# Kernel optimization log

Hardware: AMD Instinct MI355X
Metric: run time of the kernel (lower is better)

## Reference

```python
import jax, jax.numpy as jnp
import numpy as np

TAU = 2.0
EPS_COH = 1e-8
EPS_NLL = 1e-7
ALPHA = 0.0
# component-vs-modality mask: rows = (common, synergy, g_spec, p_spec), cols = (gene, path)
MASK = np.array([[1.0, 1.0], [0.0, 0.0], [1.0, 0.0], [0.0, 1.0]], dtype=np.float32)


def l2norm(x, axis=-1):
    n = jnp.sqrt(jnp.sum(x * x, axis=axis, keepdims=True))
    return x / jnp.maximum(n, 1e-12)


def setup_inputs() -> dict:
    key = jax.random.key(0)
    ks = jax.random.split(key, 8)
    B, K, C, N = 64, 4, 256, 8192
    hazards = jax.random.uniform(ks[0], (B, K), dtype=jnp.float32)
    S = jnp.cumprod(1.0 - hazards, axis=1)  # survival curve, matches torch semantics
    indiv = jax.random.normal(ks[1], (B, 4, C), dtype=jnp.float32)
    gene = jax.random.normal(ks[2], (B, 1, C), dtype=jnp.float32)
    path = jax.random.normal(ks[3], (B, 1, C), dtype=jnp.float32)
    cohort_bank = jax.random.normal(ks[4], (K, N, 4, C), dtype=jnp.float32)
    label = jax.random.randint(ks[5], (B,), 0, K).astype(jnp.int32)
    c = jax.random.randint(ks[6], (B,), 0, 2).astype(jnp.int32)
    return {"hazards": hazards, "S": S, "indiv": indiv, "gene": gene,
            "path": path, "cohort_bank": cohort_bank, "label": label, "c": c}


def reference(hazards, S, indiv, gene, path, cohort_bank, label, c):
    B, K = hazards.shape
    dt = hazards.dtype
    # ---- NLLSurvLoss ----
    cf = c.astype(dt)[:, None]                       # [B,1] censoring flag
    Y = label.astype(jnp.int32)[:, None]             # [B,1]
    S_padded = jnp.concatenate([jnp.ones((B, 1), dt), S], axis=1)  # [B,K+1]
    s_y = jnp.take_along_axis(S_padded, Y, axis=1)
    h_y = jnp.take_along_axis(hazards, Y, axis=1)
    s_y1 = jnp.take_along_axis(S_padded, Y + 1, axis=1)
    clamp = lambda x: jnp.maximum(x, EPS_NLL)
    uncensored = -(1.0 - cf) * (jnp.log(clamp(s_y)) + jnp.log(clamp(h_y)))
    censored = -cf * jnp.log(clamp(s_y1))
    neg_l = censored + uncensored
    nll = ((1.0 - ALPHA) * neg_l + ALPHA * uncensored).mean()
    # ---- CohortLoss: intra ----
    indiv_n = l2norm(indiv)                          # [B,4,C]
    gp_n = l2norm(jnp.concatenate([gene, path], axis=1))  # [B,2,C]
    sim = jnp.einsum('bpc,btc->bpt', indiv_n, gp_n)  # [B,4,2]
    mask = jnp.asarray(MASK, dtype=dt)               # [4,2]
    intra = (jnp.abs(sim) * (1.0 - mask) - mask * sim).mean(axis=(1, 2)) + 1.0
    intra_loss = intra.mean()
    # ---- CohortLoss: inter (vectorized cohort-bank retrieval) ----
    n_cls, N = cohort_bank.shape[0], cohort_bank.shape[1]
    anchors = l2norm(indiv.mean(axis=1))             # [B,C]
    bank_means = cohort_bank.mean(axis=2)            # [n_cls,N,C]
    bank_n = l2norm(bank_means)                      # [n_cls,N,C]
    sims = jnp.einsum('knc,bc->bkn', bank_n, anchors)  # [B,n_cls,N]
    e = jnp.exp(sims / TAU)
    pos_mask = (label[:, None] == jnp.arange(n_cls, dtype=label.dtype)[None, :]).astype(dt)[:, :, None]  # [B,n_cls,1]
    ep = jnp.sum(e * pos_mask) / (B * N)                       # mean over B*N positive sims
    en = jnp.sum(e * (1.0 - pos_mask)) / (B * (n_cls - 1) * N)  # mean over B*(n_cls-1)*N negative sims
    inter_loss = -jnp.log((ep + EPS_COH) / (ep + en + EPS_COH))
    cohort_loss = intra_loss + inter_loss
    # Loss_factory: total = 1.0*nllsurv + 1.0*cohort
    return nll + cohort_loss
```

## Files before the change

### kernel.cpp

```cpp
#include <hip/hip_runtime.h>
#include <math.h>

#define BB 64
#define KK 4
#define CC 256
#define NN 8192
#define NROWS (KK*NN)
#define GRID_NORM 2048
#define GRID_INTER 512
#define WPG 4

#define WS_BN_OFF    0
#define WS_B_OFF     16777216
#define WS_SLOT_OFF  16809984
#define WS_NLL_OFF   16818176
#define WS_INTRA_OFF 16818432
#define WS_TKT_OFF   16818688

#define EPS_NLL 1e-7f

typedef __attribute__((ext_vector_type(8))) short bf16x8;
typedef __attribute__((ext_vector_type(4))) float f32x4;

__device__ __forceinline__ float4 f4add(float4 a, float4 b){ return make_float4(a.x+b.x, a.y+b.y, a.z+b.z, a.w+b.w); }
__device__ __forceinline__ float4 f4scale(float4 a, float s){ return make_float4(a.x*s, a.y*s, a.z*s, a.w*s); }
__device__ __forceinline__ float dot4(float4 a, float4 b){ return a.x*b.x + a.y*b.y + a.z*b.z + a.w*b.w; }

__device__ __forceinline__ float wred(float v){
#pragma unroll
  for (int m = 32; m >= 1; m >>= 1) v += __shfl_xor(v, m, 64);
  return v;
}

__device__ __forceinline__ unsigned short f2bf(float x){
  union { float f; unsigned u; } v; v.f = x;
  unsigned r = v.u + 0x7fffu + ((v.u >> 16) & 1u);
  return (unsigned short)(r >> 16);
}

__global__ __launch_bounds__(64) void prep_kernel(
    const float* __restrict__ hazards, const float* __restrict__ S,
    const float* __restrict__ indiv,   const float* __restrict__ gene,
    const float* __restrict__ path,    const int* __restrict__ label,
    const int* __restrict__ cvec,      char* __restrict__ ws)
{
  const int b = blockIdx.x;
  const int lane = threadIdx.x;

  const float4* ind4 = (const float4*)indiv + (size_t)b * 256;
  float4 i0 = ind4[  0 + lane];
  float4 i1 = ind4[ 64 + lane];
  float4 i2 = ind4[128 + lane];
  float4 i3 = ind4[192 + lane];
  float4 g  = ((const float4*)gene)[b*64 + lane];
  float4 p  = ((const float4*)path)[b*64 + lane];

  float4 am = f4scale(f4add(f4add(i0, i1), f4add(i2, i3)), 0.25f);
  float na = sqrtf(wred(dot4(am, am)));
  float4 an = f4scale(am, 1.0f / fmaxf(na, 1e-12f));

  {
    const int cq = lane;
    const unsigned addr = (unsigned)((cq >> 3) * 4096
                        + (b >> 4) * 1024
                        + ((((cq >> 1) & 3) * 16) + (b & 15)) * 16
                        + (cq & 1) * 8);
    ushort4 h4;
    h4.x = f2bf(an.x); h4.y = f2bf(an.y); h4.z = f2bf(an.z); h4.w = f2bf(an.w);
    *(ushort4*)(ws + WS_B_OFF + addr) = h4;
  }

  float4 v[6] = {i0, i1, i2, i3, g, p};
#pragma unroll
  for (int j = 0; j < 6; ++j) {
    float n = sqrtf(wred(dot4(v[j], v[j])));
    v[j] = f4scale(v[j], 1.0f / fmaxf(n, 1e-12f));
  }

  float s[4][2];
#pragma unroll
  for (int pp = 0; pp < 4; ++pp)
#pragma unroll
    for (int t = 0; t < 2; ++t)
      s[pp][t] = wred(dot4(v[pp], v[4+t]));

  if (lane == 0) {
    float intra = (-s[0][0]) + (-s[0][1])
                + fabsf(s[1][0]) + fabsf(s[1][1])
                + (-s[2][0]) + fabsf(s[2][1])
                + fabsf(s[3][0]) + (-s[3][1]);
    intra = intra * 0.125f + 1.0f;
    ((float*)(ws + WS_INTRA_OFF))[b] = intra;

    int   Y  = label[b];
    float cf = (float)cvec[b];
    float s_y  = (Y == 0) ? 1.0f : S[b*KK + Y - 1];
    float s_y1 = S[b*KK + Y];
    float h_y  = hazards[b*KK + Y];
    float neg_l = -cf * logf(fmaxf(s_y1, EPS_NLL))
                  - (1.0f - cf) * (logf(fmaxf(s_y, EPS_NLL)) + logf(fmaxf(h_y, EPS_NLL)));
    ((float*)(ws + WS_NLL_OFF))[b] = neg_l;
  }
}

__global__ __launch_bounds__(256, 4) void bank_norm_kernel(
    const float* __restrict__ bank, char* __restrict__ ws)
{
  const int tid  = threadIdx.x;
  const int wave = tid >> 6;
  const int lane = tid & 63;
  const int gw   = blockIdx.x * WPG + wave;
  const int row0 = gw * 4;

  const float4* b4 = (const float4*)bank;
  ushort4* bn = (ushort4*)(ws + WS_BN_OFF);

  float4 r[4][4];
#pragma unroll
  for (int rr = 0; rr < 4; ++rr)
#pragma unroll
    for (int c = 0; c < 4; ++c)
      r[rr][c] = b4[(size_t)(row0 + rr) * 256 + c * 64 + lane];

#pragma unroll
  for (int rr = 0; rr < 4; ++rr) {
    float4 m = f4add(f4add(r[rr][0], r[rr][1]), f4add(r[rr][2], r[rr][3]));
    float ss = wred(dot4(m, m));
    float rs = rsqrtf(fmaxf(ss, 1e-24f));
    ushort4 h4;
    h4.x = f2bf(m.x * rs); h4.y = f2bf(m.y * rs);
    h4.z = f2bf(m.z * rs); h4.w = f2bf(m.w * rs);
    bn[(size_t)(row0 + rr) * 64 + lane] = h4;
  }
}

__global__ __launch_bounds__(256) void inter_kernel(
    const int* __restrict__ label, char* __restrict__ ws, float* __restrict__ out)
{
  __shared__ uint4 Bl[2048];
  __shared__ double redw[WPG][2];
  __shared__ unsigned tkt_s;

  const int tid  = threadIdx.x;
  const int wave = tid >> 6;
  const int lane = tid & 63;
  const int lm   = lane & 15;
  const int lg   = lane >> 4;

  const uint4* Bg = (const uint4*)(ws + WS_B_OFF);
#pragma unroll
  for (int i = 0; i < 8; ++i) Bl[tid + i*256] = Bg[tid + i*256];
  __syncthreads();

  const int gw   = blockIdx.x * WPG + wave;
  const int row0 = gw * 16;
  const int kk   = row0 >> 13;

  int lab[4];
#pragma unroll
  for (int nt = 0; nt < 4; ++nt) lab[nt] = label[nt*16 + lm];

  const short* bnp = (const short*)(ws + WS_BN_OFF) + (size_t)(row0 + lm) * 256 + lg * 8;
  bf16x8 af[8];
#pragma unroll
  for (int kc = 0; kc < 8; ++kc)
    af[kc] = *(const bf16x8*)(bnp + kc * 32);

  f32x4 acc0 = {0,0,0,0}, acc1 = {0,0,0,0}, acc2 = {0,0,0,0}, acc3 = {0,0,0,0};
#pragma unroll
  for (int kc = 0; kc < 8; ++kc) {
    acc0 = __builtin_amdgcn_mfma_f32_16x16x32_bf16(af[kc], *(const bf16x8*)&Bl[(kc*4+0)*64 + lane], acc0, 0, 0, 0);
    acc1 = __builtin_amdgcn_mfma_f32_16x16x32_bf16(af[kc], *(const bf16x8*)&Bl[(kc*4+1)*64 + lane], acc1, 0, 0, 0);
    acc2 = __builtin_amdgcn_mfma_f32_16x16x32_bf16(af[kc], *(const bf16x8*)&Bl[(kc*4+2)*64 + lane], acc2, 0, 0, 0);
    acc3 = __builtin_amdgcn_mfma_f32_16x16x32_bf16(af[kc], *(const bf16x8*)&Bl[(kc*4+3)*64 + lane], acc3, 0, 0, 0);
  }

  float epf = 0.0f, enf = 0.0f;
#define DO_NT(ACC, NT)                                                        \
  {                                                                           \
    float es = expf(ACC.x * 0.5f) + expf(ACC.y * 0.5f)                        \
             + expf(ACC.z * 0.5f) + expf(ACC.w * 0.5f);                       \
    if (lab[NT] == kk) epf += es; else enf += es;                             \
  }
  DO_NT(acc0, 0) DO_NT(acc1, 1) DO_NT(acc2, 2) DO_NT(acc3, 3)
#undef DO_NT

  epf = wred(epf);
  enf = wred(enf);
  if (lane == 0) {
    redw[wave][0] = (double)epf;
    redw[wave][1] = (double)enf;
  }
  __syncthreads();

  double*   slots  = (double*)(ws + WS_SLOT_OFF);
  unsigned* ticket = (unsigned*)(ws + WS_TKT_OFF);

  if (tid == 0) {
    double bep = 0.0, ben = 0.0;
#pragma unroll
    for (int w = 0; w < WPG; ++w) { bep += redw[w][0]; ben += redw[w][1]; }
    slots[blockIdx.x*2 + 0] = bep;
    slots[blockIdx.x*2 + 1] = ben;
    __threadfence();
    tkt_s = atomicAdd(ticket, 1u);
  }
  __syncthreads();

  if (tkt_s == GRID_INTER - 1 && wave == 0) {
    __threadfence();
    double pep = 0.0, pen = 0.0;
    for (int i = lane; i < GRID_INTER; i += 64) {
      pep += slots[2*i + 0];
      pen += slots[2*i + 1];
    }
#pragma unroll
    for (int m = 32; m >= 1; m >>= 1) {
      pep += __shfl_xor(pep, m, 64);
      pen += __shfl_xor(pen, m, 64);
    }
    float scal = ((const float*)(ws + WS_NLL_OFF))[lane]
               + ((const float*)(ws + WS_INTRA_OFF))[lane];
    scal = wred(scal);
    if (lane == 0) {
      double ep = pep / (double)(BB * NN);
      double en = pen / (double)(BB * (KK-1) * NN);
      double inter = -log((ep + 1e-8) / (ep + en + 1e-8));
      out[0] = (float)((double)scal / 64.0 + inter);
    }
  }
}

extern "C" void kernel_launch(void* const* d_in, const int* in_sizes, int n_in,
                              void* d_out, int out_size, void* d_ws, size_t ws_size,
                              hipStream_t stream)
{
  const float* hazards = (const float*)d_in[0];
  const float* S       = (const float*)d_in[1];
  const float* indiv   = (const float*)d_in[2];
  const float* gene    = (const float*)d_in[3];
  const float* path    = (const float*)d_in[4];
  const float* bank    = (const float*)d_in[5];
  const int*   label   = (const int*)d_in[6];
  const int*   cvec    = (const int*)d_in[7];
  char*  ws  = (char*)d_ws;
  float* out = (float*)d_out;

  hipMemsetAsync(ws + WS_TKT_OFF, 0, 4, stream);
  prep_kernel<<<dim3(BB), dim3(64), 0, stream>>>(hazards, S, indiv, gene, path, label, cvec, ws);
  bank_norm_kernel<<<dim3(GRID_NORM), dim3(256), 0, stream>>>(bank, ws);
  inter_kernel<<<dim3(GRID_INTER), dim3(256), 0, stream>>>(label, ws, out);
}
```

Measured before the change: 229.7 us.

## Fuse bank normalization into inter kernel via per-wave LDS staging

Merges the cohort-bank mean/normalize pass into the MFMA similarity kernel. Each wave loads 16 bank rows in four passes, normalizes them and writes bf16 into a swizzled per-wave LDS tile, which then feeds the MFMA A operand directly. This drops the 16 MB bf16 intermediate write and re-read plus one kernel launch. In exchange, only 512 blocks must stream the 128 MB bank, with more LDS per block and an occupancy hint of 2, which may reduce memory-level parallelism.

```diff
diff --git a/kernel.cpp b/kernel.cpp
--- a/kernel.cpp
+++ b/kernel.cpp
@@ -6,16 +6,14 @@
 #define CC 256
 #define NN 8192
 #define NROWS (KK*NN)
-#define GRID_NORM 2048
-#define GRID_INTER 512
+#define GRID_F 512
 #define WPG 4
 
-#define WS_BN_OFF    0
-#define WS_B_OFF     16777216
-#define WS_SLOT_OFF  16809984
-#define WS_NLL_OFF   16818176
-#define WS_INTRA_OFF 16818432
-#define WS_TKT_OFF   16818688
+#define WS_B_OFF     0
+#define WS_SLOT_OFF  32768
+#define WS_NLL_OFF   40960
+#define WS_INTRA_OFF 41216
+#define WS_TKT_OFF   41472
 
 #define EPS_NLL 1e-7f
 
@@ -103,41 +101,12 @@
   }
 }
 
-__global__ __launch_bounds__(256, 4) void bank_norm_kernel(
-    const float* __restrict__ bank, char* __restrict__ ws)
-{
-  const int tid  = threadIdx.x;
-  const int wave = tid >> 6;
-  const int lane = tid & 63;
-  const int gw   = blockIdx.x * WPG + wave;
-  const int row0 = gw * 4;
-
-  const float4* b4 = (const float4*)bank;
-  ushort4* bn = (ushort4*)(ws + WS_BN_OFF);
-
-  float4 r[4][4];
-#pragma unroll
-  for (int rr = 0; rr < 4; ++rr)
-#pragma unroll
-    for (int c = 0; c < 4; ++c)
-      r[rr][c] = b4[(size_t)(row0 + rr) * 256 + c * 64 + lane];
-
-#pragma unroll
-  for (int rr = 0; rr < 4; ++rr) {
-    float4 m = f4add(f4add(r[rr][0], r[rr][1]), f4add(r[rr][2], r[rr][3]));
-    float ss = wred(dot4(m, m));
-    float rs = rsqrtf(fmaxf(ss, 1e-24f));
-    ushort4 h4;
-    h4.x = f2bf(m.x * rs); h4.y = f2bf(m.y * rs);
-    h4.z = f2bf(m.z * rs); h4.w = f2bf(m.w * rs);
-    bn[(size_t)(row0 + rr) * 64 + lane] = h4;
-  }
-}
-
-__global__ __launch_bounds__(256) void inter_kernel(
-    const int* __restrict__ label, char* __restrict__ ws, float* __restrict__ out)
+__global__ __launch_bounds__(256, 2) void fused_kernel(
+    const float* __restrict__ bank, const int* __restrict__ label,
+    char* __restrict__ ws, float* __restrict__ out)
 {
   __shared__ uint4 Bl[2048];
+  __shared__ uint4 At4[WPG][512];
   __shared__ double redw[WPG][2];
   __shared__ unsigned tkt_s;
 
@@ -155,16 +124,42 @@
   const int gw   = blockIdx.x * WPG + wave;
   const int row0 = gw * 16;
   const int kk   = row0 >> 13;
+  char* At = (char*)&At4[wave][0];
 
   int lab[4];
 #pragma unroll
   for (int nt = 0; nt < 4; ++nt) lab[nt] = label[nt*16 + lm];
 
-  const short* bnp = (const short*)(ws + WS_BN_OFF) + (size_t)(row0 + lm) * 256 + lg * 8;
+  const float4* b4 = (const float4*)bank;
+
+#pragma unroll 1
+  for (int pass = 0; pass < 4; ++pass) {
+    const int rp0 = row0 + pass * 4;
+
+    float4 r[4][4];
+#pragma unroll
+    for (int rr = 0; rr < 4; ++rr)
+#pragma unroll
+      for (int c = 0; c < 4; ++c)
+        r[rr][c] = b4[(size_t)(rp0 + rr) * 256 + c * 64 + lane];
+
+#pragma unroll
+    for (int rr = 0; rr < 4; ++rr) {
+      float4 m = f4add(f4add(r[rr][0], r[rr][1]), f4add(r[rr][2], r[rr][3]));
+      float ss = wred(dot4(m, m));
+      float rs = rsqrtf(fmaxf(ss, 1e-24f));
+      const int lr = pass * 4 + rr;
+      ushort4 h4;
+      h4.x = f2bf(m.x * rs); h4.y = f2bf(m.y * rs);
+      h4.z = f2bf(m.z * rs); h4.w = f2bf(m.w * rs);
+      *(ushort4*)(At + lr*512 + ((lane*8) ^ ((lr & 7) << 4))) = h4;
+    }
+  }
+
   bf16x8 af[8];
 #pragma unroll
   for (int kc = 0; kc < 8; ++kc)
-    af[kc] = *(const bf16x8*)(bnp + kc * 32);
+    af[kc] = *(const bf16x8*)(At + lm*512 + ((kc*64 + lg*16) ^ ((lm & 7) << 4)));
 
   f32x4 acc0 = {0,0,0,0}, acc1 = {0,0,0,0}, acc2 = {0,0,0,0}, acc3 = {0,0,0,0};
 #pragma unroll
@@ -207,10 +202,10 @@
   }
   __syncthreads();
 
-  if (tkt_s == GRID_INTER - 1 && wave == 0) {
+  if (tkt_s == GRID_F - 1 && wave == 0) {
     __threadfence();
     double pep = 0.0, pen = 0.0;
-    for (int i = lane; i < GRID_INTER; i += 64) {
+    for (int i = lane; i < GRID_F; i += 64) {
       pep += slots[2*i + 0];
       pen += slots[2*i + 1];
     }
@@ -248,6 +243,5 @@
 
   hipMemsetAsync(ws + WS_TKT_OFF, 0, 4, stream);
   prep_kernel<<<dim3(BB), dim3(64), 0, stream>>>(hazards, S, indiv, gene, path, label, cvec, ws);
-  bank_norm_kernel<<<dim3(GRID_NORM), dim3(256), 0, stream>>>(bank, ws);
-  inter_kernel<<<dim3(GRID_INTER), dim3(256), 0, stream>>>(label, ws, out);
-}
+  fused_kernel<<<dim3(GRID_F), dim3(256), 0, stream>>>(bank, label, ws, out);
+}
```

New measurement: 234.5 us. 2.1% more time.

## Write normalized bank in MFMA-fragment layout and halve rows per wave

Applied to the files above, without the earlier changes.

The bank normalization kernel now handles two rows per wave instead of four, doubles its grid and raises the occupancy hint. It stores the bf16 normalized rows in a tiled layout that matches the MFMA A-fragment order. The inter kernel can then read each fragment as a contiguous 16-byte-per-lane load instead of strided row reads. The intent is more memory parallelism in the bandwidth-bound 128MB bank read and coalesced fragment loads in the GEMM stage.

```diff
diff --git a/kernel.cpp b/kernel.cpp
--- a/kernel.cpp
+++ b/kernel.cpp
@@ -6,7 +6,7 @@
 #define CC 256
 #define NN 8192
 #define NROWS (KK*NN)
-#define GRID_NORM 2048
+#define GRID_NORM 4096
 #define GRID_INTER 512
 #define WPG 4
 
@@ -103,35 +103,48 @@
   }
 }
 
-__global__ __launch_bounds__(256, 4) void bank_norm_kernel(
+__global__ __launch_bounds__(256, 8) void norm_stream_kernel(
     const float* __restrict__ bank, char* __restrict__ ws)
 {
   const int tid  = threadIdx.x;
   const int wave = tid >> 6;
   const int lane = tid & 63;
   const int gw   = blockIdx.x * WPG + wave;
-  const int row0 = gw * 4;
+  const int row0 = gw * 2;
 
   const float4* b4 = (const float4*)bank;
-  ushort4* bn = (ushort4*)(ws + WS_BN_OFF);
-
-  float4 r[4][4];
-#pragma unroll
-  for (int rr = 0; rr < 4; ++rr)
-#pragma unroll
-    for (int c = 0; c < 4; ++c)
-      r[rr][c] = b4[(size_t)(row0 + rr) * 256 + c * 64 + lane];
-
-#pragma unroll
-  for (int rr = 0; rr < 4; ++rr) {
-    float4 m = f4add(f4add(r[rr][0], r[rr][1]), f4add(r[rr][2], r[rr][3]));
-    float ss = wred(dot4(m, m));
-    float rs = rsqrtf(fmaxf(ss, 1e-24f));
-    ushort4 h4;
-    h4.x = f2bf(m.x * rs); h4.y = f2bf(m.y * rs);
-    h4.z = f2bf(m.z * rs); h4.w = f2bf(m.w * rs);
-    bn[(size_t)(row0 + rr) * 64 + lane] = h4;
-  }
+
+  float4 r0[4], r1[4];
+#pragma unroll
+  for (int c = 0; c < 4; ++c) r0[c] = b4[(size_t)row0       * 256 + c * 64 + lane];
+#pragma unroll
+  for (int c = 0; c < 4; ++c) r1[c] = b4[(size_t)(row0 + 1) * 256 + c * 64 + lane];
+
+  float4 m0 = f4add(f4add(r0[0], r0[1]), f4add(r0[2], r0[3]));
+  float4 m1 = f4add(f4add(r1[0], r1[1]), f4add(r1[2], r1[3]));
+  float s0 = dot4(m0, m0);
+  float s1 = dot4(m1, m1);
+#pragma unroll
+  for (int sh = 32; sh >= 1; sh >>= 1) {
+    s0 += __shfl_xor(s0, sh, 64);
+    s1 += __shfl_xor(s1, sh, 64);
+  }
+  const float q0 = rsqrtf(fmaxf(s0, 1e-24f));
+  const float q1 = rsqrtf(fmaxf(s1, 1e-24f));
+
+  const unsigned lanedest = (unsigned)((lane >> 3) * 1024
+                          + ((lane >> 1) & 3) * 256
+                          + (lane & 1) * 8);
+  const int t0 = row0 >> 4,        lm0 = row0 & 15;
+  const int t1 = (row0 + 1) >> 4,  lm1 = (row0 + 1) & 15;
+
+  ushort4 h0, h1;
+  h0.x = f2bf(m0.x * q0); h0.y = f2bf(m0.y * q0);
+  h0.z = f2bf(m0.z * q0); h0.w = f2bf(m0.w * q0);
+  h1.x = f2bf(m1.x * q1); h1.y = f2bf(m1.y * q1);
+  h1.z = f2bf(m1.z * q1); h1.w = f2bf(m1.w * q1);
+  *(ushort4*)(ws + WS_BN_OFF + (size_t)t0 * 8192 + lanedest + lm0 * 16) = h0;
+  *(ushort4*)(ws + WS_BN_OFF + (size_t)t1 * 8192 + lanedest + lm1 * 16) = h1;
 }
 
 __global__ __launch_bounds__(256) void inter_kernel(
@@ -145,7 +158,6 @@
   const int wave = tid >> 6;
   const int lane = tid & 63;
   const int lm   = lane & 15;
-  const int lg   = lane >> 4;
 
   const uint4* Bg = (const uint4*)(ws + WS_B_OFF);
 #pragma unroll
@@ -153,18 +165,17 @@
   __syncthreads();
 
   const int gw   = blockIdx.x * WPG + wave;
-  const int row0 = gw * 16;
-  const int kk   = row0 >> 13;
+  const int kk   = (gw * 16) >> 13;
 
   int lab[4];
 #pragma unroll
   for (int nt = 0; nt < 4; ++nt) lab[nt] = label[nt*16 + lm];
 
-  const short* bnp = (const short*)(ws + WS_BN_OFF) + (size_t)(row0 + lm) * 256 + lg * 8;
+  const char* bnp = ws + WS_BN_OFF + (size_t)gw * 8192;
   bf16x8 af[8];
 #pragma unroll
   for (int kc = 0; kc < 8; ++kc)
-    af[kc] = *(const bf16x8*)(bnp + kc * 32);
+    af[kc] = *(const bf16x8*)(bnp + kc * 1024 + lane * 16);
 
   f32x4 acc0 = {0,0,0,0}, acc1 = {0,0,0,0}, acc2 = {0,0,0,0}, acc3 = {0,0,0,0};
 #pragma unroll
@@ -248,6 +259,6 @@
 
   hipMemsetAsync(ws + WS_TKT_OFF, 0, 4, stream);
   prep_kernel<<<dim3(BB), dim3(64), 0, stream>>>(hazards, S, indiv, gene, path, label, cvec, ws);
-  bank_norm_kernel<<<dim3(GRID_NORM), dim3(256), 0, stream>>>(bank, ws);
+  norm_stream_kernel<<<dim3(GRID_NORM), dim3(256), 0, stream>>>(bank, ws);
   inter_kernel<<<dim3(GRID_INTER), dim3(256), 0, stream>>>(label, ws, out);
 }
```

New measurement: 228.4 us. No clear change (-0.6%).
